# Kernel tuning notes

Measured on AMD Instinct MI355X. Metric: run time of the kernel, lower is better.

## Reference

```python
import jax, jax.numpy as jnp
import numpy as np

# irreps multiplicities: node = NSx0e + NVx1o, edge = ESx0e + EVx1o, hidden = HSx0e + HVx1o
NS, NV = 64, 32
ES, EV = 8, 8
HS, HV = 96, 32          # Gate splits HS scalars -> (HS-HV) silu scalars + HV sigmoid gates
N_NODES, N_EDGES = 10000, 100000
INV_SQRT3 = float(1.0 / np.sqrt(3.0))  # w3j(1,1,0) coefficient


def _split(x, ns, nv):
    # [N, ns + 3*nv] -> scalars [N, ns], vectors [N, nv, 3]
    return x[:, :ns], x[:, ns:].reshape(x.shape[0], nv, 3)


def _merge(s, v):
    return jnp.concatenate([s, v.reshape(v.shape[0], -1)], axis=-1)


def _fc_tp(xs, xv, ys, yv, w_ss, w_vv, w_sv, w_vs):
    """FullyConnectedTensorProduct for l<=1 irreps with path ('element') normalization.
    Paths: 0e*0e->0e, 1o*1o->0e (dot/sqrt3), 0e*1o->1o, 1o*0e->1o."""
    fan_s = w_ss.shape[0] * w_ss.shape[1] + w_vv.shape[0] * w_vv.shape[1]
    fan_v = w_sv.shape[0] * w_sv.shape[1] + w_vs.shape[0] * w_vs.shape[1]
    out_s = (jnp.einsum('eu,ev,uvw->ew', xs, ys, w_ss)
             + INV_SQRT3 * jnp.einsum('eum,evm,uvw->ew', xv, yv, w_vv)) / np.sqrt(fan_s)
    out_v = (jnp.einsum('eu,evm,uvw->ewm', xs, yv, w_sv)
             + jnp.einsum('eum,ev,uvw->ewm', xv, ys, w_vs)) / np.sqrt(fan_v)
    return out_s, out_v


def _gate(s, v, n_plain):
    # e3nn Gate: silu on plain scalars, sigmoid gates multiply each vector channel
    plain = jax.nn.silu(s[:, :n_plain])
    gates = jax.nn.sigmoid(s[:, n_plain:])
    return plain, v * gates[:, :, None]


def _lin(s, v, Ws, Wv):
    # e3nn equivariant Linear: mixes multiplicities per irrep, shared over m, 1/sqrt(fan_in)
    return (s @ Ws) / np.sqrt(Ws.shape[0]), jnp.einsum('num,uw->nwm', v, Wv) / np.sqrt(Wv.shape[0])


def setup_inputs() -> dict:
    key = jax.random.key(0)
    ks = jax.random.split(key, 15)
    rn = lambda k, sh: jax.random.normal(k, sh, dtype=jnp.float32)
    return {
        'node_features': rn(ks[0], (N_NODES, NS + 3 * NV)),
        'edge_attr': rn(ks[1], (N_EDGES, ES + 3 * EV)),
        'w_msg_ss': rn(ks[2], (NS, ES, HS)),
        'w_msg_vv': rn(ks[3], (NV, EV, HS)),
        'w_msg_sv': rn(ks[4], (NS, EV, HV)),
        'w_msg_vs': rn(ks[5], (NV, ES, HV)),
        'w_lin_msg_s': rn(ks[6], (HS - HV, HS)),
        'w_lin_msg_v': rn(ks[7], (HV, HV)),
        'w_upd_ss': rn(ks[8], (NS, HS, HS)),
        'w_upd_vv': rn(ks[9], (NV, HV, HS)),
        'w_upd_sv': rn(ks[10], (NS, HV, HV)),
        'w_upd_vs': rn(ks[11], (NV, HS, HV)),
        'w_lin_upd_s': rn(ks[12], (HS - HV, NS)),
        'w_lin_upd_v': rn(ks[13], (HV, NV)),
        'edge_index': jax.random.randint(ks[14], (2, N_EDGES), 0, N_NODES),
    }


def reference(node_features, edge_attr, w_msg_ss, w_msg_vv, w_msg_sv, w_msg_vs,
              w_lin_msg_s, w_lin_msg_v, w_upd_ss, w_upd_vv, w_upd_sv, w_upd_vs,
              w_lin_upd_s, w_lin_upd_v, edge_index):
    row, col = edge_index[0], edge_index[1]
    ns, nv = _split(node_features, NS, NV)
    es, ev = _split(edge_attr, ES, EV)

    # messages: gather -> CG tensor product -> gate -> linear
    ms, mv = _fc_tp(ns[col], nv[col], es, ev, w_msg_ss, w_msg_vv, w_msg_sv, w_msg_vs)
    ps, pv = _gate(ms, mv, HS - HV)                  # [E, HS-HV], [E, HV, 3]
    ls, lv = _lin(ps, pv, w_lin_msg_s, w_lin_msg_v)  # [E, HS],    [E, HV, 3]

    # scatter-sum aggregation onto destination nodes
    agg_s = jax.ops.segment_sum(ls, row, num_segments=N_NODES)
    agg_v = jax.ops.segment_sum(lv, row, num_segments=N_NODES)

    # node update: CG tensor product with aggregated messages -> gate -> linear -> residual
    us, uv = _fc_tp(ns, nv, agg_s, agg_v, w_upd_ss, w_upd_vv, w_upd_sv, w_upd_vs)
    gs, gv = _gate(us, uv, HS - HV)
    ds, dv = _lin(gs, gv, w_lin_upd_s, w_lin_upd_v)  # [N, NS], [N, NV, 3]
    return _merge(ns + ds, nv + dv)
```

## Files before the change

kernel.cpp:

```cpp
#include <hip/hip_runtime.h>
#include <hip/hip_bf16.h>

constexpr int kNodes = 10000;
constexpr int kEdges = 100000;

constexpr float INV_SQRT3    = 0.57735026918962576f;
constexpr float INV_SQRT768  = 0.036084391824351615f;
constexpr float INV_SQRT7168 = 0.011811389781538352f;
constexpr float INV_SQRT5120 = 0.013975424859373686f;
constexpr float INV_SQRT32   = 0.17677669529663687f;

constexpr size_t MSGW_OFF  = 0;
constexpr size_t UPDW1_OFF = 196608;
constexpr size_t UPDW2_OFF = 1572864;
constexpr size_t MLINS_OFF = 1900544;
constexpr size_t MLINV_OFF = 1912832;
constexpr size_t ULINS_OFF = 1914880;
constexpr size_t ULINV_OFF = 1923072;
constexpr size_t CNT_OFF   = 1926144;
constexpr size_t CUR_OFF   = 1967104;
constexpr size_t PERM_OFF  = 2008064;

typedef __attribute__((ext_vector_type(8))) short bf8;
typedef __attribute__((ext_vector_type(4))) float f4;
union BF { bf8 v; short s[8]; unsigned u[4]; };

__device__ __forceinline__ short f2bf(float f) {
    union { float f; unsigned u; } c; c.f = f;
    unsigned r = c.u + 0x7fffu + ((c.u >> 16) & 1u);
    return (short)(r >> 16);
}
__device__ __forceinline__ unsigned pk2(float lo, float hi) {
    union { __hip_bfloat162 h; unsigned u; } c;
    c.h = __float22bfloat162_rn(make_float2(lo, hi));
    return c.u;
}
__device__ __forceinline__ f4 mfma16(bf8 a, bf8 b, f4 c) {
    return __builtin_amdgcn_mfma_f32_16x16x32_bf16(a, b, c, 0, 0, 0);
}
__device__ __forceinline__ bf8 ldB(const char* p) {
    return *(const bf8*)p;
}
__device__ __forceinline__ float fsig(float x) { return 1.0f / (1.0f + __expf(-x)); }

__global__ void prep_kernel(
    const float* __restrict__ Wmss, const float* __restrict__ Wmvv,
    const float* __restrict__ Wmsv, const float* __restrict__ Wmvs,
    const float* __restrict__ Wlms, const float* __restrict__ Wlmv,
    const float* __restrict__ Wuss, const float* __restrict__ Wuvv,
    const float* __restrict__ Wusv, const float* __restrict__ Wuvs,
    const float* __restrict__ Wlus, const float* __restrict__ Wluv,
    char* __restrict__ wout)
{
    int i = blockIdx.x * 256 + threadIdx.x;
    float v;
    short* dst;
    if (i < 98304) {
        dst = (short*)(wout + MSGW_OFF) + i;
        int t = i >> 12, q = i & 4095, r = q >> 5, c = q & 31;
        int k = t * 32 + c;
        if (r < 96) {
            v = (k < 512 ? Wmss[k * 96 + r]
                         : Wmvv[(k - 512) * 96 + r] * INV_SQRT3) * INV_SQRT768;
        } else {
            int n2 = r - 96;
            if (k < 512) { int u = k & 63, vv = k >> 6; v = Wmsv[(u * 8 + vv) * 32 + n2] * INV_SQRT768; }
            else         { v = Wmvs[(k - 512) * 32 + n2] * INV_SQRT768; }
        }
    } else if (i < 786432) {
        int j = i - 98304;
        dst = (short*)(wout + UPDW1_OFF) + j;
        int t = j / 3072, q = j % 3072, r = q >> 5, c = q & 31;
        int k = t * 32 + c;
        if (k < 6144) { int u = k & 63, vv = k >> 6;
            v = Wuss[(u * 96 + vv) * 96 + r] * INV_SQRT7168; }
        else { int r2 = k - 6144; int u = r2 & 31, vv = r2 >> 5;
            v = Wuvv[(u * 32 + vv) * 96 + r] * (INV_SQRT3 * INV_SQRT7168); }
    } else if (i < 950272) {
        int j = i - 786432;
        dst = (short*)(wout + UPDW2_OFF) + j;
        int t = j >> 10, q = j & 1023, r = q >> 5, c = q & 31;
        int k = t * 32 + c;
        if (k < 2048) { int u = k & 63, vv = k >> 6;
            v = Wusv[(u * 32 + vv) * 32 + r] * INV_SQRT5120; }
        else { int r2 = k - 2048;
            v = Wuvs[r2 * 32 + r] * INV_SQRT5120; }
    } else if (i < 956416) {
        int j = i - 950272;
        dst = (short*)(wout + MLINS_OFF) + j;
        int n = j >> 6, kk = j & 63;
        v = Wlms[kk * 96 + n] * 0.125f;
    } else if (i < 957440) {
        int j = i - 956416;
        dst = (short*)(wout + MLINV_OFF) + j;
        int n = j >> 5, kk = j & 31;
        v = Wlmv[kk * 32 + n] * INV_SQRT32;
    } else if (i < 961536) {
        int j = i - 957440;
        dst = (short*)(wout + ULINS_OFF) + j;
        int n = j >> 6, kk = j & 63;
        v = Wlus[kk * 64 + n] * 0.125f;
    } else if (i < 962560) {
        int j = i - 961536;
        dst = (short*)(wout + ULINV_OFF) + j;
        int n = j >> 5, kk = j & 31;
        v = Wluv[kk * 32 + n] * INV_SQRT32;
    } else return;
    *dst = f2bf(v);
}

__global__ __launch_bounds__(256) void hist_kernel(const int* __restrict__ eidx,
                                                   int* __restrict__ cnt)
{
    int e = blockIdx.x * 256 + threadIdx.x;
    if (e < kEdges) atomicAdd(&cnt[eidx[e]], 1);
}

__global__ __launch_bounds__(256) void scan_kernel(const int* __restrict__ cnt,
                                                   int* __restrict__ cursor)
{
    __shared__ int psum[256];
    const int t = threadIdx.x, base = t * 40;
    int s = 0;
    for (int j = 0; j < 40; ++j) { int idx = base + j; if (idx < kNodes) s += cnt[idx]; }
    psum[t] = s;
    __syncthreads();
    if (t == 0) { int a = 0; for (int i = 0; i < 256; ++i) { int x = psum[i]; psum[i] = a; a += x; } }
    __syncthreads();
    int run = psum[t];
    for (int j = 0; j < 40; ++j) {
        int idx = base + j;
        if (idx < kNodes) { cursor[idx] = run; run += cnt[idx]; }
    }
}

__global__ __launch_bounds__(256) void scatter_kernel(const int* __restrict__ eidx,
                                                      int* __restrict__ cursor,
                                                      int* __restrict__ perm)
{
    int e = blockIdx.x * 256 + threadIdx.x;
    if (e < kEdges) {
        int p = atomicAdd(&cursor[eidx[e]], 1);
        perm[p] = e;
    }
}

__global__ __launch_bounds__(256, 3) void msg_kernel(
    const float* __restrict__ nf, const float* __restrict__ ea,
    const int* __restrict__ eidx, const char* __restrict__ wout,
    float* __restrict__ agg)
{
    __shared__ char pool[42752];
    float* nf_sh   = (float*)pool;
    float* ea_sh   = (float*)(pool + 20992);
    float* aggloc  = (float*)pool;
    int*   row_sh  = (int*)  (pool + 25600);
    int*   rank_sh = (int*)  (pool + 25728);
    float* gat     = (float*)(pool + 25856);
    short* silu_s  = (short*)(pool + 30464);
    short* pv_s    = (short*)(pool + 35072);

    const int t = threadIdx.x, w = t >> 6, lane = t & 63;
    const int l15 = lane & 15, lg = lane >> 4;
    const int eblk = blockIdx.x * 32;

    const char* msgW = wout + MSGW_OFF;
    const int*  perm = (const int*)(wout + PERM_OFF);

    {
        const int i = t >> 3, j = t & 7;
        const int pe = perm[eblk + i];
        if (j == 0) row_sh[i] = eidx[pe];
        const int col = eidx[kEdges + pe];
        const float4* src = (const float4*)(nf + (size_t)col * 160);
        for (int c = j; c < 40; c += 8) *(float4*)&nf_sh[i * 164 + c * 4] = src[c];
        const float4* esrc = (const float4*)(ea + (size_t)pe * 32);
        *(float4*)&ea_sh[i * 36 + j * 4] = esrc[j];
    }
    __syncthreads();

    f4 accS[3] = {{0.f,0.f,0.f,0.f},{0.f,0.f,0.f,0.f},{0.f,0.f,0.f,0.f}};
    f4 accV[3] = {{0.f,0.f,0.f,0.f},{0.f,0.f,0.f,0.f},{0.f,0.f,0.f,0.f}};
    const int Ms = w >> 1, nb = (w & 1) * 3;
    const int es_ = Ms * 16 + l15;

    const float4 ey0 = *(const float4*)&ea_sh[es_ * 36];
    const float4 ey1 = *(const float4*)&ea_sh[es_ * 36 + 4];
    float eyv[24];
    #pragma unroll
    for (int q = 0; q < 6; ++q)
        *(float4*)&eyv[q * 4] = *(const float4*)&ea_sh[es_ * 36 + 8 + q * 4];

    for (int kt = 0; kt < 16; ++kt) {
        const char* wb = msgW + kt * 8192;
        BF aS;
        {
            const int uu = kt * 4 + lg;
            const float xs = nf_sh[es_ * 164 + uu];
            aS.u[0] = pk2(xs * ey0.x, xs * ey0.y);
            aS.u[1] = pk2(xs * ey0.z, xs * ey0.w);
            aS.u[2] = pk2(xs * ey1.x, xs * ey1.y);
            aS.u[3] = pk2(xs * ey1.z, xs * ey1.w);
        }
        #pragma unroll
        for (int i = 0; i < 3; ++i)
            accS[i] = mfma16(aS.v, ldB(wb + ((nb + i) * 16 + l15) * 64 + lg * 16), accS[i]);

        BF aV; int prevMv = -1;
        #pragma unroll
        for (int i = 0; i < 3; ++i) {
            const int tv = 3 * w + i, Mv = tv >> 1, Nv = tv & 1;
            if (Mv != prevMv) {
                prevMv = Mv;
                const int m = Mv >> 1, ev = (Mv & 1) * 16 + l15;
                const int kp = kt * 32 + lg * 8;
                const int vv = kp >> 6, u0 = kp & 63;
                const float ym = ea_sh[ev * 36 + 8 + 3 * vv + m];
                const float4 x0 = *(const float4*)&nf_sh[ev * 164 + u0];
                const float4 x1 = *(const float4*)&nf_sh[ev * 164 + u0 + 4];
                aV.u[0] = pk2(x0.x * ym, x0.y * ym);
                aV.u[1] = pk2(x0.z * ym, x0.w * ym);
                aV.u[2] = pk2(x1.x * ym, x1.y * ym);
                aV.u[3] = pk2(x1.z * ym, x1.w * ym);
            }
            accV[i] = mfma16(aV.v, ldB(wb + (96 + (Nv * 16 + l15)) * 64 + lg * 16), accV[i]);
        }
    }
    for (int kt = 16; kt < 24; ++kt) {
        const char* wb = msgW + kt * 8192;
        BF aS;
        {
            const int uu = (kt - 16) * 4 + lg;
            const float* xp = &nf_sh[es_ * 164 + 64 + 3 * uu];
            const float x0 = xp[0], x1 = xp[1], x2 = xp[2];
            #pragma unroll
            for (int j = 0; j < 4; ++j) {
                float a0 = x0 * eyv[6*j  ] + x1 * eyv[6*j+1] + x2 * eyv[6*j+2];
                float a1 = x0 * eyv[6*j+3] + x1 * eyv[6*j+4] + x2 * eyv[6*j+5];
                aS.u[j] = pk2(a0, a1);
            }
        }
        #pragma unroll
        for (int i = 0; i < 3; ++i)
            accS[i] = mfma16(aS.v, ldB(wb + ((nb + i) * 16 + l15) * 64 + lg * 16), accS[i]);

        BF aV; int prevMv = -1;
        #pragma unroll
        for (int i = 0; i < 3; ++i) {
            const int tv = 3 * w + i, Mv = tv >> 1, Nv = tv & 1;
            if (Mv != prevMv) {
                prevMv = Mv;
                const int m = Mv >> 1, ev = (Mv & 1) * 16 + l15;
                const int uu = (kt - 16) * 4 + lg;
                const float xm = nf_sh[ev * 164 + 64 + 3 * uu + m];
                const float4 y0 = *(const float4*)&ea_sh[ev * 36];
                const float4 y1 = *(const float4*)&ea_sh[ev * 36 + 4];
                aV.u[0] = pk2(xm * y0.x, xm * y0.y);
                aV.u[1] = pk2(xm * y0.z, xm * y0.w);
                aV.u[2] = pk2(xm * y1.x, xm * y1.y);
                aV.u[3] = pk2(xm * y1.z, xm * y1.w);
            }
            accV[i] = mfma16(aV.v, ldB(wb + (96 + (Nv * 16 + l15)) * 64 + lg * 16), accV[i]);
        }
    }

    __syncthreads();

    #pragma unroll
    for (int i = 0; i < 3; ++i) {
        const int n = (nb + i) * 16 + l15;
        #pragma unroll
        for (int r = 0; r < 4; ++r) {
            const int e = Ms * 16 + lg * 4 + r;
            const float v = accS[i][r];
            if (n < 64) silu_s[e * 72 + n] = f2bf(v * fsig(v));
            else        gat[e * 36 + (n - 64)] = fsig(v);
        }
    }
    for (int idx = t; idx < 32 * 192; idx += 256) aggloc[idx] = 0.f;
    if (t < 32) {
        const int ri = row_sh[t];
        int rk = t;
        for (int j2 = 0; j2 < t; ++j2) if (row_sh[j2] == ri) { rk = j2; break; }
        rank_sh[t] = rk;
    }
    __syncthreads();

    #pragma unroll
    for (int i = 0; i < 3; ++i) {
        const int tv = 3 * w + i, Mv = tv >> 1, Nv = tv & 1;
        const int m = Mv >> 1, eb = (Mv & 1) * 16;
        const int u = Nv * 16 + l15;
        #pragma unroll
        for (int r = 0; r < 4; ++r) {
            const int e = eb + lg * 4 + r;
            pv_s[(m * 32 + e) * 40 + u] = f2bf(accV[i][r] * gat[e * 36 + u]);
        }
    }
    __syncthreads();

    {
        const char* mls = wout + MLINS_OFF;
        f4 acc[3] = {{0.f,0.f,0.f,0.f},{0.f,0.f,0.f,0.f},{0.f,0.f,0.f,0.f}};
        #pragma unroll
        for (int k0 = 0; k0 < 2; ++k0) {
            const int kg = k0 * 32 + lg * 8;
            bf8 a = *(const bf8*)&silu_s[es_ * 72 + kg];
            #pragma unroll
            for (int i = 0; i < 3; ++i)
                acc[i] = mfma16(a, ldB(mls + ((nb + i) * 16 + l15) * 128 + kg * 2), acc[i]);
        }
        #pragma unroll
        for (int i = 0; i < 3; ++i) {
            const int n = (nb + i) * 16 + l15;
            #pragma unroll
            for (int r = 0; r < 4; ++r) {
                const int e = Ms * 16 + lg * 4 + r;
                atomicAdd(&aggloc[rank_sh[e] * 192 + n], acc[i][r]);
            }
        }
    }
    {
        const char* mlv = wout + MLINV_OFF;
        f4 acc[3] = {{0.f,0.f,0.f,0.f},{0.f,0.f,0.f,0.f},{0.f,0.f,0.f,0.f}};
        const int kg = lg * 8;
        BF a; int prevMv = -1;
        #pragma unroll
        for (int i = 0; i < 3; ++i) {
            const int tv = 3 * w + i, Mv = tv >> 1, Nv = tv & 1;
            if (Mv != prevMv) { prevMv = Mv; a.v = *(const bf8*)&pv_s[(Mv * 16 + l15) * 40 + kg]; }
            acc[i] = mfma16(a.v, ldB(mlv + (Nv * 16 + l15) * 64 + kg * 2), acc[i]);
        }
        #pragma unroll
        for (int i = 0; i < 3; ++i) {
            const int tv = 3 * w + i, Mv = tv >> 1, Nv = tv & 1;
            const int w2 = Nv * 16 + l15;
            #pragma unroll
            for (int r = 0; r < 4; ++r) {
                const int rr = Mv * 16 + lg * 4 + r;
                const int m = rr >> 5, e = rr & 31;
                atomicAdd(&aggloc[rank_sh[e] * 192 + 96 + w2 * 3 + m], acc[i][r]);
            }
        }
    }
    __syncthreads();

    for (int idx = t; idx < 32 * 192; idx += 256) {
        const int ii = idx / 192, c = idx - ii * 192;
        if (rank_sh[ii] == ii)
            atomicAdd(&agg[(size_t)row_sh[ii] * 192 + c], aggloc[idx]);
    }
}

__global__ __launch_bounds__(512, 4) void upd_kernel(
    const float* __restrict__ nf, const char* __restrict__ wout,
    float* __restrict__ agg)
{
    __shared__ float nf_sh[32 * 164];
    __shared__ float ag_sh[32 * 196];
    __shared__ float gat[32 * 36];
    __shared__ short silu_s[32 * 72];
    __shared__ short gv_s[96 * 40];
    __shared__ float red[3072];

    const int t = threadIdx.x, w = t >> 6, lane = t & 63;
    const int g = w >> 2, wl = w & 3;
    const int l15 = lane & 15, lg = lane >> 4;
    const int nblk = blockIdx.x * 32;
    const char* W1 = wout + UPDW1_OFF;
    const char* W2 = wout + UPDW2_OFF;

    {
        const int i = t >> 4, j = t & 15;
        int n = nblk + i; if (n > kNodes - 1) n = kNodes - 1;
        const float4* src = (const float4*)(nf + (size_t)n * 160);
        for (int c = j; c < 40; c += 16) *(float4*)&nf_sh[i * 164 + c * 4] = src[c];
        const float4* asrc = (const float4*)(agg + (size_t)n * 192);
        for (int c = j; c < 48; c += 16) *(float4*)&ag_sh[i * 196 + c * 4] = asrc[c];
    }
    __syncthreads();

    const int Ms = wl >> 1, nb = (wl & 1) * 3;
    const int es_ = Ms * 16 + l15;

    f4 accS[3] = {{0.f,0.f,0.f,0.f},{0.f,0.f,0.f,0.f},{0.f,0.f,0.f,0.f}};
    {
        const int kt0 = g * 112, kt1 = kt0 + 112;
        const int ktSS = kt1 < 192 ? kt1 : 192;
        int kt = kt0;
        for (; kt < ktSS; ++kt) {
            const char* wb = W1 + (size_t)kt * 6144;
            const int kp = kt * 32 + lg * 8;
            const int vv = kp >> 6, u0 = kp & 63;
            const float ys = ag_sh[es_ * 196 + vv];
            const float4 x0 = *(const float4*)&nf_sh[es_ * 164 + u0];
            const float4 x1 = *(const float4*)&nf_sh[es_ * 164 + u0 + 4];
            BF aS;
            aS.u[0] = pk2(x0.x * ys, x0.y * ys);
            aS.u[1] = pk2(x0.z * ys, x0.w * ys);
            aS.u[2] = pk2(x1.x * ys, x1.y * ys);
            aS.u[3] = pk2(x1.z * ys, x1.w * ys);
            #pragma unroll
            for (int i = 0; i < 3; ++i)
                accS[i] = mfma16(aS.v, ldB(wb + ((nb + i) * 16 + l15) * 64 + lg * 16), accS[i]);
        }
        for (; kt < kt1; ++kt) {
            const char* wb = W1 + (size_t)kt * 6144;
            const int rp = kt * 32 + lg * 8 - 6144;
            const int vv = rp >> 5, u0 = rp & 31;
            const float* xp = &nf_sh[es_ * 164 + 64 + 3 * u0];
            const float* gp = &ag_sh[es_ * 196 + 96 + 3 * vv];
            const float g0 = gp[0], g1 = gp[1], g2 = gp[2];
            BF aS;
            #pragma unroll
            for (int j = 0; j < 4; ++j) {
                float a0 = xp[6*j  ] * g0 + xp[6*j+1] * g1 + xp[6*j+2] * g2;
                float a1 = xp[6*j+3] * g0 + xp[6*j+4] * g1 + xp[6*j+5] * g2;
                aS.u[j] = pk2(a0, a1);
            }
            #pragma unroll
            for (int i = 0; i < 3; ++i)
                accS[i] = mfma16(aS.v, ldB(wb + ((nb + i) * 16 + l15) * 64 + lg * 16), accS[i]);
        }
    }

    if (g == 1) {
        #pragma unroll
        for (int i = 0; i < 3; ++i) {
            const int n = (nb + i) * 16 + l15;
            #pragma unroll
            for (int r = 0; r < 4; ++r)
                red[(Ms * 16 + lg * 4 + r) * 96 + n] = accS[i][r];
        }
    }
    __syncthreads();
    if (g == 0) {
        #pragma unroll
        for (int i = 0; i < 3; ++i) {
            const int n = (nb + i) * 16 + l15;
            #pragma unroll
            for (int r = 0; r < 4; ++r) {
                const int e = Ms * 16 + lg * 4 + r;
                const float v = accS[i][r] + red[e * 96 + n];
                if (n < 64) silu_s[e * 72 + n] = f2bf(v * fsig(v));
                else        gat[e * 36 + (n - 64)] = fsig(v);
            }
        }
    }
    __syncthreads();

    f4 accV[3] = {{0.f,0.f,0.f,0.f},{0.f,0.f,0.f,0.f},{0.f,0.f,0.f,0.f}};
    {
        const int kt0 = g * 80, kt1 = kt0 + 80;
        const int ktSV = kt1 < 64 ? kt1 : 64;
        int kt = kt0;
        for (; kt < ktSV; ++kt) {
            const char* wb = W2 + (size_t)kt * 2048;
            BF aV; int prevMv = -1;
            #pragma unroll
            for (int i = 0; i < 3; ++i) {
                const int tv = 3 * wl + i, Mv = tv >> 1, Nv = tv & 1;
                if (Mv != prevMv) {
                    prevMv = Mv;
                    const int m = Mv >> 1, ev = (Mv & 1) * 16 + l15;
                    const int kp = kt * 32 + lg * 8;
                    const int vv = kp >> 6, u0 = kp & 63;
                    const float ym = ag_sh[ev * 196 + 96 + 3 * vv + m];
                    const float4 x0 = *(const float4*)&nf_sh[ev * 164 + u0];
                    const float4 x1 = *(const float4*)&nf_sh[ev * 164 + u0 + 4];
                    aV.u[0] = pk2(x0.x * ym, x0.y * ym);
                    aV.u[1] = pk2(x0.z * ym, x0.w * ym);
                    aV.u[2] = pk2(x1.x * ym, x1.y * ym);
                    aV.u[3] = pk2(x1.z * ym, x1.w * ym);
                }
                accV[i] = mfma16(aV.v, ldB(wb + (Nv * 16 + l15) * 64 + lg * 16), accV[i]);
            }
        }
        for (; kt < kt1; ++kt) {
            const char* wb = W2 + (size_t)kt * 2048;
            BF aV; int prevMv = -1;
            #pragma unroll
            for (int i = 0; i < 3; ++i) {
                const int tv = 3 * wl + i, Mv = tv >> 1, Nv = tv & 1;
                if (Mv != prevMv) {
                    prevMv = Mv;
                    const int m = Mv >> 1, ev = (Mv & 1) * 16 + l15;
                    const int rp = kt * 32 + lg * 8 - 2048;
                    const int u = rp / 96, v0 = rp - u * 96;
                    const float xm = nf_sh[ev * 164 + 64 + 3 * u + m];
                    const float4 y0 = *(const float4*)&ag_sh[ev * 196 + v0];
                    const float4 y1 = *(const float4*)&ag_sh[ev * 196 + v0 + 4];
                    aV.u[0] = pk2(xm * y0.x, xm * y0.y);
                    aV.u[1] = pk2(xm * y0.z, xm * y0.w);
                    aV.u[2] = pk2(xm * y1.x, xm * y1.y);
                    aV.u[3] = pk2(xm * y1.z, xm * y1.w);
                }
                accV[i] = mfma16(aV.v, ldB(wb + (Nv * 16 + l15) * 64 + lg * 16), accV[i]);
            }
        }
    }

    if (g == 1) {
        #pragma unroll
        for (int i = 0; i < 3; ++i) {
            const int tv = 3 * wl + i, Mv = tv >> 1, Nv = tv & 1;
            #pragma unroll
            for (int r = 0; r < 4; ++r)
                red[(Mv * 16 + lg * 4 + r) * 32 + Nv * 16 + l15] = accV[i][r];
        }
    }
    __syncthreads();
    if (g == 0) {
        #pragma unroll
        for (int i = 0; i < 3; ++i) {
            const int tv = 3 * wl + i, Mv = tv >> 1, Nv = tv & 1;
            const int m = Mv >> 1, eb = (Mv & 1) * 16;
            const int u = Nv * 16 + l15;
            #pragma unroll
            for (int r = 0; r < 4; ++r) {
                const int e = eb + lg * 4 + r;
                const float v = accV[i][r] + red[(Mv * 16 + lg * 4 + r) * 32 + u];
                gv_s[(m * 32 + e) * 40 + u] = f2bf(v * gat[e * 36 + u]);
            }
        }
    }
    __syncthreads();

    const int nvalid = kNodes - nblk;
    if (g == 0) {
        {
            const char* uls = wout + ULINS_OFF;
            f4 acc[2] = {{0.f,0.f,0.f,0.f},{0.f,0.f,0.f,0.f}};
            const int nb2 = (wl & 1) * 2;
            #pragma unroll
            for (int k0 = 0; k0 < 2; ++k0) {
                const int kg = k0 * 32 + lg * 8;
                bf8 a = *(const bf8*)&silu_s[es_ * 72 + kg];
                #pragma unroll
                for (int i = 0; i < 2; ++i)
                    acc[i] = mfma16(a, ldB(uls + ((nb2 + i) * 16 + l15) * 128 + kg * 2), acc[i]);
            }
            #pragma unroll
            for (int i = 0; i < 2; ++i) {
                const int n = (nb2 + i) * 16 + l15;
                #pragma unroll
                for (int r = 0; r < 4; ++r) {
                    const int e = Ms * 16 + lg * 4 + r;
                    if (e < nvalid)
                        agg[(size_t)(nblk + e) * 192 + n] = nf_sh[e * 164 + n] + acc[i][r];
                }
            }
        }
        {
            const char* ulv = wout + ULINV_OFF;
            f4 acc[3] = {{0.f,0.f,0.f,0.f},{0.f,0.f,0.f,0.f},{0.f,0.f,0.f,0.f}};
            const int kg = lg * 8;
            BF a; int prevMv = -1;
            #pragma unroll
            for (int i = 0; i < 3; ++i) {
                const int tv = 3 * wl + i, Mv = tv >> 1, Nv = tv & 1;
                if (Mv != prevMv) { prevMv = Mv; a.v = *(const bf8*)&gv_s[(Mv * 16 + l15) * 40 + kg]; }
                acc[i] = mfma16(a.v, ldB(ulv + (Nv * 16 + l15) * 64 + kg * 2), acc[i]);
            }
            #pragma unroll
            for (int i = 0; i < 3; ++i) {
                const int tv = 3 * wl + i, Mv = tv >> 1, Nv = tv & 1;
                const int w2 = Nv * 16 + l15;
                #pragma unroll
                for (int r = 0; r < 4; ++r) {
                    const int rr = Mv * 16 + lg * 4 + r;
                    const int m = rr >> 5, e = rr & 31;
                    if (e < nvalid)
                        agg[(size_t)(nblk + e) * 192 + 64 + w2 * 3 + m]
                            = nf_sh[e * 164 + 64 + w2 * 3 + m] + acc[i][r];
                }
            }
        }
    }
}

__global__ __launch_bounds__(256) void copy_kernel(const float* __restrict__ agg,
                                                   float* __restrict__ out)
{
    int i = blockIdx.x * 256 + threadIdx.x;
    if (i < 400000) {
        int n = i / 40, c = i - n * 40;
        ((float4*)out)[i] = ((const float4*)agg)[n * 48 + c];
    }
}

extern "C" void kernel_launch(void* const* d_in, const int* in_sizes, int n_in,
                              void* d_out, int out_size, void* d_ws, size_t ws_size,
                              hipStream_t stream) {
    const float* nf   = (const float*)d_in[0];
    const float* ea   = (const float*)d_in[1];
    const int*   eidx = (const int*)d_in[14];
    float* agg = (float*)d_ws;
    char*  wout = (char*)d_out;

    hipMemsetAsync(agg, 0, 7680000, stream);
    hipMemsetAsync(wout + CNT_OFF, 0, 40960, stream);
    prep_kernel<<<3760, 256, 0, stream>>>(
        (const float*)d_in[2], (const float*)d_in[3], (const float*)d_in[4],
        (const float*)d_in[5], (const float*)d_in[6], (const float*)d_in[7],
        (const float*)d_in[8], (const float*)d_in[9], (const float*)d_in[10],
        (const float*)d_in[11], (const float*)d_in[12], (const float*)d_in[13], wout);
    hist_kernel<<<391, 256, 0, stream>>>(eidx, (int*)(wout + CNT_OFF));
    scan_kernel<<<1, 256, 0, stream>>>((const int*)(wout + CNT_OFF), (int*)(wout + CUR_OFF));
    scatter_kernel<<<391, 256, 0, stream>>>(eidx, (int*)(wout + CUR_OFF), (int*)(wout + PERM_OFF));
    msg_kernel<<<kEdges / 32, 256, 0, stream>>>(nf, ea, eidx, wout, agg);
    upd_kernel<<<(kNodes + 31) / 32, 512, 0, stream>>>(nf, wout, agg);
    copy_kernel<<<1563, 256, 0, stream>>>(agg, (float*)d_out);
}
```

Before: 524.9 us.

## Process 64 edges per msg block with bf16 node staging and run-based local aggregation

The message kernel now handles 64 sorted edges per block instead of 32. It loads the weight B fragments once per k-step and reuses them across two M-tiles, which halves weight traffic per edge. Node features are staged in shared memory as bf16 so the larger tile fits, and the gate values are stored as bf16. Local aggregation now uses run-length ranks capped at 24 distinct destination rows, with overflow rows sent straight to global atomics. The trade-offs are higher register and LDS use, which may cut occupancy, and an extra bf16 rounding of node inputs that changes numerics slightly.

```diff
diff --git a/kernel.cpp b/kernel.cpp
--- a/kernel.cpp
+++ b/kernel.cpp
@@ -34,6 +34,9 @@
     union { __hip_bfloat162 h; unsigned u; } c;
     c.h = __float22bfloat162_rn(make_float2(lo, hi));
     return c.u;
+}
+__device__ __forceinline__ float bf2f(unsigned short s) {
+    union { float f; unsigned u; } c; c.u = ((unsigned)s) << 16; return c.f;
 }
 __device__ __forceinline__ f4 mfma16(bf8 a, bf8 b, f4 c) {
     return __builtin_amdgcn_mfma_f32_16x16x32_bf16(a, b, c, 0, 0, 0);
@@ -150,205 +153,243 @@
     const int* __restrict__ eidx, const char* __restrict__ wout,
     float* __restrict__ agg)
 {
-    __shared__ char pool[42752];
-    float* nf_sh   = (float*)pool;
-    float* ea_sh   = (float*)(pool + 20992);
-    float* aggloc  = (float*)pool;
-    int*   row_sh  = (int*)  (pool + 25600);
-    int*   rank_sh = (int*)  (pool + 25728);
-    float* gat     = (float*)(pool + 25856);
-    short* silu_s  = (short*)(pool + 30464);
-    short* pv_s    = (short*)(pool + 35072);
+    __shared__ char pool[49792];
+    unsigned short* nf_bf = (unsigned short*)pool;
+    float* ea_sh  = (float*)(pool + 21504);
+    short* silu_s = (short*)pool;
+    short* gat    = (short*)(pool + 9216);
+    short* pv_s   = (short*)(pool + 14336);
+    float* aggloc = (float*)(pool + 30720);
+    int*   row_sh = (int*)(pool + 49152);
+    int*   rank_sh= (int*)(pool + 49408);
+    int*   rrow   = (int*)(pool + 49664);
+    int*   nh_sh  = (int*)(pool + 49760);
 
     const int t = threadIdx.x, w = t >> 6, lane = t & 63;
     const int l15 = lane & 15, lg = lane >> 4;
-    const int eblk = blockIdx.x * 32;
+    const int eblk = blockIdx.x * 64;
 
     const char* msgW = wout + MSGW_OFF;
     const int*  perm = (const int*)(wout + PERM_OFF);
 
     {
-        const int i = t >> 3, j = t & 7;
-        const int pe = perm[eblk + i];
+        const int i = t >> 2, j = t & 3;
+        const bool valid = (eblk + i) < kEdges;
+        const int pe = perm[valid ? eblk + i : kEdges - 1];
         if (j == 0) row_sh[i] = eidx[pe];
         const int col = eidx[kEdges + pe];
         const float4* src = (const float4*)(nf + (size_t)col * 160);
-        for (int c = j; c < 40; c += 8) *(float4*)&nf_sh[i * 164 + c * 4] = src[c];
+        for (int c = j; c < 40; c += 4) {
+            float4 v4 = src[c];
+            *(uint2*)&nf_bf[i * 168 + c * 4] = make_uint2(pk2(v4.x, v4.y), pk2(v4.z, v4.w));
+        }
         const float4* esrc = (const float4*)(ea + (size_t)pe * 32);
-        *(float4*)&ea_sh[i * 36 + j * 4] = esrc[j];
-    }
-    __syncthreads();
-
-    f4 accS[3] = {{0.f,0.f,0.f,0.f},{0.f,0.f,0.f,0.f},{0.f,0.f,0.f,0.f}};
-    f4 accV[3] = {{0.f,0.f,0.f,0.f},{0.f,0.f,0.f,0.f},{0.f,0.f,0.f,0.f}};
+        const float4 z4 = make_float4(0.f, 0.f, 0.f, 0.f);
+        *(float4*)&ea_sh[i * 36 + j * 8]     = valid ? esrc[j * 2]     : z4;
+        *(float4*)&ea_sh[i * 36 + j * 8 + 4] = valid ? esrc[j * 2 + 1] : z4;
+    }
+    __syncthreads();
+
+    f4 accS[2][3] = {}; f4 accV[2][3] = {};
     const int Ms = w >> 1, nb = (w & 1) * 3;
-    const int es_ = Ms * 16 + l15;
-
-    const float4 ey0 = *(const float4*)&ea_sh[es_ * 36];
-    const float4 ey1 = *(const float4*)&ea_sh[es_ * 36 + 4];
-    float eyv[24];
+    float4 ey0[2], ey1[2];
     #pragma unroll
-    for (int q = 0; q < 6; ++q)
-        *(float4*)&eyv[q * 4] = *(const float4*)&ea_sh[es_ * 36 + 8 + q * 4];
+    for (int m = 0; m < 2; ++m) {
+        const int es = m * 32 + Ms * 16 + l15;
+        ey0[m] = *(const float4*)&ea_sh[es * 36];
+        ey1[m] = *(const float4*)&ea_sh[es * 36 + 4];
+    }
 
     for (int kt = 0; kt < 16; ++kt) {
         const char* wb = msgW + kt * 8192;
-        BF aS;
-        {
+        bf8 bs[3], bv[3];
+        #pragma unroll
+        for (int i = 0; i < 3; ++i) {
+            bs[i] = ldB(wb + ((nb + i) * 16 + l15) * 64 + lg * 16);
+            bv[i] = ldB(wb + (96 + (((3 * w + i) & 1) * 16 + l15)) * 64 + lg * 16);
+        }
+        #pragma unroll
+        for (int m = 0; m < 2; ++m) {
+            const int es = m * 32 + Ms * 16 + l15;
             const int uu = kt * 4 + lg;
-            const float xs = nf_sh[es_ * 164 + uu];
-            aS.u[0] = pk2(xs * ey0.x, xs * ey0.y);
-            aS.u[1] = pk2(xs * ey0.z, xs * ey0.w);
-            aS.u[2] = pk2(xs * ey1.x, xs * ey1.y);
-            aS.u[3] = pk2(xs * ey1.z, xs * ey1.w);
-        }
-        #pragma unroll
-        for (int i = 0; i < 3; ++i)
-            accS[i] = mfma16(aS.v, ldB(wb + ((nb + i) * 16 + l15) * 64 + lg * 16), accS[i]);
-
-        BF aV; int prevMv = -1;
-        #pragma unroll
-        for (int i = 0; i < 3; ++i) {
-            const int tv = 3 * w + i, Mv = tv >> 1, Nv = tv & 1;
-            if (Mv != prevMv) {
-                prevMv = Mv;
-                const int m = Mv >> 1, ev = (Mv & 1) * 16 + l15;
-                const int kp = kt * 32 + lg * 8;
-                const int vv = kp >> 6, u0 = kp & 63;
-                const float ym = ea_sh[ev * 36 + 8 + 3 * vv + m];
-                const float4 x0 = *(const float4*)&nf_sh[ev * 164 + u0];
-                const float4 x1 = *(const float4*)&nf_sh[ev * 164 + u0 + 4];
-                aV.u[0] = pk2(x0.x * ym, x0.y * ym);
-                aV.u[1] = pk2(x0.z * ym, x0.w * ym);
-                aV.u[2] = pk2(x1.x * ym, x1.y * ym);
-                aV.u[3] = pk2(x1.z * ym, x1.w * ym);
-            }
-            accV[i] = mfma16(aV.v, ldB(wb + (96 + (Nv * 16 + l15)) * 64 + lg * 16), accV[i]);
+            const float xs = bf2f(nf_bf[es * 168 + uu]);
+            BF aS;
+            aS.u[0] = pk2(xs * ey0[m].x, xs * ey0[m].y);
+            aS.u[1] = pk2(xs * ey0[m].z, xs * ey0[m].w);
+            aS.u[2] = pk2(xs * ey1[m].x, xs * ey1[m].y);
+            aS.u[3] = pk2(xs * ey1[m].z, xs * ey1[m].w);
+            #pragma unroll
+            for (int i = 0; i < 3; ++i) accS[m][i] = mfma16(aS.v, bs[i], accS[m][i]);
+
+            BF aV; int prevMv = -1;
+            #pragma unroll
+            for (int i = 0; i < 3; ++i) {
+                const int tv = 3 * w + i, Mv = tv >> 1;
+                if (Mv != prevMv) {
+                    prevMv = Mv;
+                    const int mc = Mv >> 1, ev = m * 32 + (Mv & 1) * 16 + l15;
+                    const int kp = kt * 32 + lg * 8;
+                    const int vv = kp >> 6, u0 = kp & 63;
+                    const float ym = ea_sh[ev * 36 + 8 + 3 * vv + mc];
+                    const uint4 xq = *(const uint4*)&nf_bf[ev * 168 + u0];
+                    aV.u[0] = pk2(__uint_as_float(xq.x << 16) * ym, __uint_as_float(xq.x & 0xffff0000u) * ym);
+                    aV.u[1] = pk2(__uint_as_float(xq.y << 16) * ym, __uint_as_float(xq.y & 0xffff0000u) * ym);
+                    aV.u[2] = pk2(__uint_as_float(xq.z << 16) * ym, __uint_as_float(xq.z & 0xffff0000u) * ym);
+                    aV.u[3] = pk2(__uint_as_float(xq.w << 16) * ym, __uint_as_float(xq.w & 0xffff0000u) * ym);
+                }
+                accV[m][i] = mfma16(aV.v, bv[i], accV[m][i]);
+            }
         }
     }
     for (int kt = 16; kt < 24; ++kt) {
         const char* wb = msgW + kt * 8192;
-        BF aS;
-        {
-            const int uu = (kt - 16) * 4 + lg;
-            const float* xp = &nf_sh[es_ * 164 + 64 + 3 * uu];
-            const float x0 = xp[0], x1 = xp[1], x2 = xp[2];
+        bf8 bs[3], bv[3];
+        #pragma unroll
+        for (int i = 0; i < 3; ++i) {
+            bs[i] = ldB(wb + ((nb + i) * 16 + l15) * 64 + lg * 16);
+            bv[i] = ldB(wb + (96 + (((3 * w + i) & 1) * 16 + l15)) * 64 + lg * 16);
+        }
+        const int uu = (kt - 16) * 4 + lg;
+        #pragma unroll
+        for (int m = 0; m < 2; ++m) {
+            const int es = m * 32 + Ms * 16 + l15;
+            const float x0 = bf2f(nf_bf[es * 168 + 64 + 3 * uu]);
+            const float x1 = bf2f(nf_bf[es * 168 + 64 + 3 * uu + 1]);
+            const float x2 = bf2f(nf_bf[es * 168 + 64 + 3 * uu + 2]);
+            float ey_[24];
+            #pragma unroll
+            for (int q = 0; q < 6; ++q)
+                *(float4*)&ey_[q * 4] = *(const float4*)&ea_sh[es * 36 + 8 + q * 4];
+            BF aS;
             #pragma unroll
             for (int j = 0; j < 4; ++j) {
-                float a0 = x0 * eyv[6*j  ] + x1 * eyv[6*j+1] + x2 * eyv[6*j+2];
-                float a1 = x0 * eyv[6*j+3] + x1 * eyv[6*j+4] + x2 * eyv[6*j+5];
+                float a0 = x0 * ey_[6*j  ] + x1 * ey_[6*j+1] + x2 * ey_[6*j+2];
+                float a1 = x0 * ey_[6*j+3] + x1 * ey_[6*j+4] + x2 * ey_[6*j+5];
                 aS.u[j] = pk2(a0, a1);
             }
-        }
-        #pragma unroll
-        for (int i = 0; i < 3; ++i)
-            accS[i] = mfma16(aS.v, ldB(wb + ((nb + i) * 16 + l15) * 64 + lg * 16), accS[i]);
-
-        BF aV; int prevMv = -1;
+            #pragma unroll
+            for (int i = 0; i < 3; ++i) accS[m][i] = mfma16(aS.v, bs[i], accS[m][i]);
+
+            BF aV; int prevMv = -1;
+            #pragma unroll
+            for (int i = 0; i < 3; ++i) {
+                const int tv = 3 * w + i, Mv = tv >> 1;
+                if (Mv != prevMv) {
+                    prevMv = Mv;
+                    const int mc = Mv >> 1, ev = m * 32 + (Mv & 1) * 16 + l15;
+                    const float xm = bf2f(nf_bf[ev * 168 + 64 + 3 * uu + mc]);
+                    const float4 y0 = *(const float4*)&ea_sh[ev * 36];
+                    const float4 y1 = *(const float4*)&ea_sh[ev * 36 + 4];
+                    aV.u[0] = pk2(xm * y0.x, xm * y0.y);
+                    aV.u[1] = pk2(xm * y0.z, xm * y0.w);
+                    aV.u[2] = pk2(xm * y1.x, xm * y1.y);
+                    aV.u[3] = pk2(xm * y1.z, xm * y1.w);
+                }
+                accV[m][i] = mfma16(aV.v, bv[i], accV[m][i]);
+            }
+        }
+    }
+
+    __syncthreads();
+
+    #pragma unroll
+    for (int m = 0; m < 2; ++m)
+        #pragma unroll
+        for (int i = 0; i < 3; ++i) {
+            const int n = (nb + i) * 16 + l15;
+            #pragma unroll
+            for (int r = 0; r < 4; ++r) {
+                const int em = m * 32 + Ms * 16 + lg * 4 + r;
+                const float v = accS[m][i][r];
+                if (n < 64) silu_s[em * 72 + n] = f2bf(v * fsig(v));
+                else        gat[em * 40 + (n - 64)] = f2bf(fsig(v));
+            }
+        }
+    for (int idx = t; idx < 24 * 192; idx += 256) aggloc[idx] = 0.f;
+    if (t == 0) {
+        int nh = 0, prev = -1, cur = -1;
+        for (int i2 = 0; i2 < 64; ++i2) {
+            const int r = row_sh[i2];
+            if (r != prev) { cur = (nh < 24) ? nh : -1; if (cur >= 0) rrow[cur] = r; ++nh; prev = r; }
+            rank_sh[i2] = cur;
+        }
+        nh_sh[0] = (nh < 24) ? nh : 24;
+    }
+    __syncthreads();
+
+    #pragma unroll
+    for (int m = 0; m < 2; ++m)
         #pragma unroll
         for (int i = 0; i < 3; ++i) {
             const int tv = 3 * w + i, Mv = tv >> 1, Nv = tv & 1;
-            if (Mv != prevMv) {
-                prevMv = Mv;
-                const int m = Mv >> 1, ev = (Mv & 1) * 16 + l15;
-                const int uu = (kt - 16) * 4 + lg;
-                const float xm = nf_sh[ev * 164 + 64 + 3 * uu + m];
-                const float4 y0 = *(const float4*)&ea_sh[ev * 36];
-                const float4 y1 = *(const float4*)&ea_sh[ev * 36 + 4];
-                aV.u[0] = pk2(xm * y0.x, xm * y0.y);
-                aV.u[1] = pk2(xm * y0.z, xm * y0.w);
-                aV.u[2] = pk2(xm * y1.x, xm * y1.y);
-                aV.u[3] = pk2(xm * y1.z, xm * y1.w);
-            }
-            accV[i] = mfma16(aV.v, ldB(wb + (96 + (Nv * 16 + l15)) * 64 + lg * 16), accV[i]);
-        }
-    }
-
-    __syncthreads();
-
-    #pragma unroll
-    for (int i = 0; i < 3; ++i) {
-        const int n = (nb + i) * 16 + l15;
-        #pragma unroll
-        for (int r = 0; r < 4; ++r) {
-            const int e = Ms * 16 + lg * 4 + r;
-            const float v = accS[i][r];
-            if (n < 64) silu_s[e * 72 + n] = f2bf(v * fsig(v));
-            else        gat[e * 36 + (n - 64)] = fsig(v);
-        }
-    }
-    for (int idx = t; idx < 32 * 192; idx += 256) aggloc[idx] = 0.f;
-    if (t < 32) {
-        const int ri = row_sh[t];
-        int rk = t;
-        for (int j2 = 0; j2 < t; ++j2) if (row_sh[j2] == ri) { rk = j2; break; }
-        rank_sh[t] = rk;
-    }
-    __syncthreads();
-
-    #pragma unroll
-    for (int i = 0; i < 3; ++i) {
-        const int tv = 3 * w + i, Mv = tv >> 1, Nv = tv & 1;
-        const int m = Mv >> 1, eb = (Mv & 1) * 16;
-        const int u = Nv * 16 + l15;
-        #pragma unroll
-        for (int r = 0; r < 4; ++r) {
-            const int e = eb + lg * 4 + r;
-            pv_s[(m * 32 + e) * 40 + u] = f2bf(accV[i][r] * gat[e * 36 + u]);
-        }
-    }
+            const int mc = Mv >> 1, eb = (Mv & 1) * 16;
+            const int u = Nv * 16 + l15;
+            #pragma unroll
+            for (int r = 0; r < 4; ++r) {
+                const int em = m * 32 + eb + lg * 4 + r;
+                pv_s[(mc * 64 + em) * 40 + u] = f2bf(accV[m][i][r] * bf2f(gat[em * 40 + u]));
+            }
+        }
     __syncthreads();
 
     {
         const char* mls = wout + MLINS_OFF;
-        f4 acc[3] = {{0.f,0.f,0.f,0.f},{0.f,0.f,0.f,0.f},{0.f,0.f,0.f,0.f}};
+        f4 acc[6] = {};
         #pragma unroll
         for (int k0 = 0; k0 < 2; ++k0) {
             const int kg = k0 * 32 + lg * 8;
-            bf8 a = *(const bf8*)&silu_s[es_ * 72 + kg];
-            #pragma unroll
-            for (int i = 0; i < 3; ++i)
-                acc[i] = mfma16(a, ldB(mls + ((nb + i) * 16 + l15) * 128 + kg * 2), acc[i]);
-        }
-        #pragma unroll
-        for (int i = 0; i < 3; ++i) {
-            const int n = (nb + i) * 16 + l15;
+            #pragma unroll
+            for (int i2 = 0; i2 < 6; ++i2) {
+                const int tt = w * 6 + i2, Ms2 = tt & 3, Nn = tt >> 2;
+                bf8 a = *(const bf8*)&silu_s[(Ms2 * 16 + l15) * 72 + kg];
+                acc[i2] = mfma16(a, ldB(mls + (Nn * 16 + l15) * 128 + kg * 2), acc[i2]);
+            }
+        }
+        #pragma unroll
+        for (int i2 = 0; i2 < 6; ++i2) {
+            const int tt = w * 6 + i2, Ms2 = tt & 3, Nn = tt >> 2;
+            const int n = Nn * 16 + l15;
             #pragma unroll
             for (int r = 0; r < 4; ++r) {
-                const int e = Ms * 16 + lg * 4 + r;
-                atomicAdd(&aggloc[rank_sh[e] * 192 + n], acc[i][r]);
+                const int e64 = Ms2 * 16 + lg * 4 + r;
+                const int ri = rank_sh[e64];
+                if (ri >= 0) atomicAdd(&aggloc[ri * 192 + n], acc[i2][r]);
+                else         atomicAdd(&agg[(size_t)row_sh[e64] * 192 + n], acc[i2][r]);
             }
         }
     }
     {
         const char* mlv = wout + MLINV_OFF;
-        f4 acc[3] = {{0.f,0.f,0.f,0.f},{0.f,0.f,0.f,0.f},{0.f,0.f,0.f,0.f}};
+        f4 acc[6] = {};
         const int kg = lg * 8;
         BF a; int prevMv = -1;
         #pragma unroll
-        for (int i = 0; i < 3; ++i) {
-            const int tv = 3 * w + i, Mv = tv >> 1, Nv = tv & 1;
-            if (Mv != prevMv) { prevMv = Mv; a.v = *(const bf8*)&pv_s[(Mv * 16 + l15) * 40 + kg]; }
-            acc[i] = mfma16(a.v, ldB(mlv + (Nv * 16 + l15) * 64 + kg * 2), acc[i]);
-        }
-        #pragma unroll
-        for (int i = 0; i < 3; ++i) {
-            const int tv = 3 * w + i, Mv = tv >> 1, Nv = tv & 1;
-            const int w2 = Nv * 16 + l15;
+        for (int i2 = 0; i2 < 6; ++i2) {
+            const int tt = w * 6 + i2, Mv2 = tt >> 1, Nv2 = tt & 1;
+            if (Mv2 != prevMv) { prevMv = Mv2; a.v = *(const bf8*)&pv_s[(Mv2 * 16 + l15) * 40 + kg]; }
+            acc[i2] = mfma16(a.v, ldB(mlv + (Nv2 * 16 + l15) * 64 + kg * 2), acc[i2]);
+        }
+        #pragma unroll
+        for (int i2 = 0; i2 < 6; ++i2) {
+            const int tt = w * 6 + i2, Mv2 = tt >> 1, Nv2 = tt & 1;
+            const int w2 = Nv2 * 16 + l15;
             #pragma unroll
             for (int r = 0; r < 4; ++r) {
-                const int rr = Mv * 16 + lg * 4 + r;
-                const int m = rr >> 5, e = rr & 31;
-                atomicAdd(&aggloc[rank_sh[e] * 192 + 96 + w2 * 3 + m], acc[i][r]);
-            }
-        }
-    }
-    __syncthreads();
-
-    for (int idx = t; idx < 32 * 192; idx += 256) {
-        const int ii = idx / 192, c = idx - ii * 192;
-        if (rank_sh[ii] == ii)
-            atomicAdd(&agg[(size_t)row_sh[ii] * 192 + c], aggloc[idx]);
+                const int rr = Mv2 * 16 + lg * 4 + r;
+                const int mc = rr >> 6, e64 = rr & 63;
+                const int c = 96 + w2 * 3 + mc;
+                const int ri = rank_sh[e64];
+                if (ri >= 0) atomicAdd(&aggloc[ri * 192 + c], acc[i2][r]);
+                else         atomicAdd(&agg[(size_t)row_sh[e64] * 192 + c], acc[i2][r]);
+            }
+        }
+    }
+    __syncthreads();
+
+    const int nh = nh_sh[0];
+    for (int idx = t; idx < nh * 192; idx += 256) {
+        const int h = idx / 192, c = idx - h * 192;
+        atomicAdd(&agg[(size_t)rrow[h] * 192 + c], aggloc[h * 192 + c]);
     }
 }
 
@@ -608,7 +649,7 @@
     hist_kernel<<<391, 256, 0, stream>>>(eidx, (int*)(wout + CNT_OFF));
     scan_kernel<<<1, 256, 0, stream>>>((const int*)(wout + CNT_OFF), (int*)(wout + CUR_OFF));
     scatter_kernel<<<391, 256, 0, stream>>>(eidx, (int*)(wout + CUR_OFF), (int*)(wout + PERM_OFF));
-    msg_kernel<<<kEdges / 32, 256, 0, stream>>>(nf, ea, eidx, wout, agg);
+    msg_kernel<<<(kEdges + 63) / 64, 256, 0, stream>>>(nf, ea, eidx, wout, agg);
     upd_kernel<<<(kNodes + 31) / 32, 512, 0, stream>>>(nf, wout, agg);
     copy_kernel<<<1563, 256, 0, stream>>>(agg, (float*)d_out);
 }
```

Measured after the change: 472.5 us. 1.11x faster.
